# Performance work log

Measured on AMD Instinct MI355X. Metric: run time of the kernel, lower is better.

Reference implementation:

```python
import jax, jax.numpy as jnp
import numpy as np

CHUNK = 512  # tile size along N; keeps per-step [B,CHUNK,M] tile ~64 MB, never builds full [B,N,M]


def setup_inputs() -> dict:
    key = jax.random.key(0)
    k1, k2 = jax.random.split(key)
    xyz1 = jax.random.normal(k1, (4, 8192, 3), dtype=jnp.float32)
    xyz2 = jax.random.normal(k2, (4, 8192, 3), dtype=jnp.float32)
    return {"xyz1": xyz1, "xyz2": xyz2}


def _chamfer(xyz1, xyz2):
    # xyz1: [B,N,3], xyz2: [B,M,3]
    B, N, _ = xyz1.shape
    M = xyz2.shape[1]
    K = N // CHUNK
    x1_chunks = xyz1.reshape(B, K, CHUNK, 3).transpose(1, 0, 2, 3)  # [K,B,C,3]

    def step(carry, x1k):
        best_d2, best_i2, start = carry  # running mins for xyz2 -> xyz1 direction
        # squared distances for this tile: [B,C,M]
        d = jnp.sum((x1k[:, :, None, :] - xyz2[:, None, :, :]) ** 2, axis=-1)
        # xyz1 -> xyz2: min over M
        d1 = jnp.min(d, axis=2)                              # [B,C]
        i1 = jnp.argmin(d, axis=2).astype(jnp.int32)         # [B,C]
        # xyz2 -> xyz1: partial min over this chunk of N
        dc = jnp.min(d, axis=1)                              # [B,M]
        ic = jnp.argmin(d, axis=1).astype(jnp.int32) + start # [B,M], global index
        upd = dc < best_d2
        best_d2 = jnp.where(upd, dc, best_d2)
        best_i2 = jnp.where(upd, ic, best_i2)
        return (best_d2, best_i2, start + CHUNK), (d1, i1)

    init = (jnp.full((B, M), jnp.inf, dtype=xyz1.dtype),
            jnp.zeros((B, M), dtype=jnp.int32),
            jnp.int32(0))
    (dist2, idx2, _), (d1s, i1s) = jax.lax.scan(step, init, x1_chunks)
    dist1 = d1s.transpose(1, 0, 2).reshape(B, N)
    idx1 = i1s.transpose(1, 0, 2).reshape(B, N)
    return dist1, dist2, idx1, idx2


def reference(xyz1, xyz2):
    # Matches ChamferDistance.forward: (dist1, dist2, idx1, idx2),
    # squared nearest-neighbor distances and int32 argmin indices.
    return _chamfer(xyz1, xyz2)
```

## Files before the change

### kernel.cpp

```cpp
#include <hip/hip_runtime.h>
#include <math.h>


#define QPT 4
#define BLK 256
#define QPB (QPT*BLK)

__global__ __launch_bounds__(256, 4) void chamfer_main(
    const float* __restrict__ xyz1, const float* __restrict__ xyz2,
    unsigned long long* __restrict__ pp,
    int N, int M, int B, int S, int C)
{
    const int dir = blockIdx.z;
    const float* q = dir ? xyz2 : xyz1;
    const float* r = dir ? xyz1 : xyz2;
    const int Nq = dir ? M : N;
    const int Nr = dir ? N : M;
    const int b     = blockIdx.y / S;
    const int split = blockIdx.y % S;
    const int base  = split * C;

    extern __shared__ float s[];

    {
        const float4* gv = (const float4*)(r + ((size_t)b * Nr + base) * 3);
        float4* sv = (float4*)s;
        const int elems4 = C * 3 / 4;
        for (int t = threadIdx.x; t < elems4; t += BLK) sv[t] = gv[t];
    }
    __syncthreads();

    float qx[QPT], qy[QPT], qz[QPT];
    int qi[QPT];
    bool qv[QPT];
#pragma unroll
    for (int k = 0; k < QPT; ++k) {
        qi[k] = blockIdx.x * QPB + k * BLK + threadIdx.x;
        qv[k] = qi[k] < Nq;
        const float* qp = q + ((size_t)b * Nq + (qv[k] ? qi[k] : 0)) * 3;
        qx[k] = qp[0]; qy[k] = qp[1]; qz[k] = qp[2];
    }

    float bd[QPT];
    int   gi[QPT];
#pragma unroll
    for (int k = 0; k < QPT; ++k) { bd[k] = INFINITY; gi[k] = 0; }

    const float4* sv = (const float4*)s;
    const int iters = C / 8;
    for (int j8 = 0; j8 < iters; ++j8) {
        float4 f0 = sv[6 * j8 + 0];
        float4 f1 = sv[6 * j8 + 1];
        float4 f2 = sv[6 * j8 + 2];
        float4 f3 = sv[6 * j8 + 3];
        float4 f4 = sv[6 * j8 + 4];
        float4 f5 = sv[6 * j8 + 5];
        float px[8] = { f0.x, f0.w, f1.z, f2.y, f3.x, f3.w, f4.z, f5.y };
        float py[8] = { f0.y, f1.x, f1.w, f2.z, f3.y, f4.x, f4.w, f5.z };
        float pz[8] = { f0.z, f1.y, f2.x, f2.w, f3.z, f4.y, f5.x, f5.w };
#pragma unroll
        for (int k = 0; k < QPT; ++k) {
            float d[8];
#pragma unroll
            for (int p = 0; p < 8; ++p) {
                float dx = qx[k] - px[p];
                float dy = qy[k] - py[p];
                float dz = qz[k] - pz[p];
                d[p] = fmaf(dx, dx, fmaf(dy, dy, dz * dz));
            }
            float t0 = fminf(fminf(d[0], d[1]), d[2]);
            float t1 = fminf(fminf(d[3], d[4]), d[5]);
            float t2 = fminf(fminf(d[6], d[7]), t0);
            float m  = fminf(t1, t2);
            if (m < bd[k]) { bd[k] = m; gi[k] = j8; }
        }
    }

    const size_t obase = (size_t)(dir * B + b) * Nq;
    const int gbase = split * (C / 8);
#pragma unroll
    for (int k = 0; k < QPT; ++k) {
        if (!qv[k]) continue;
        unsigned long long packed =
            ((unsigned long long)__float_as_uint(bd[k]) << 32)
            | (unsigned)(gbase + gi[k]);
        atomicMin(&pp[obase + qi[k]], packed);
    }
}

__global__ __launch_bounds__(256) void chamfer_final(
    const float* __restrict__ xyz1, const float* __restrict__ xyz2,
    const unsigned long long* __restrict__ pp,
    float* __restrict__ out, int N, int M, int B)
{
    const int gid = blockIdx.x * blockDim.x + threadIdx.x;
    const int perDir0 = B * N;
    int dir, rem;
    if (gid < perDir0) { dir = 0; rem = gid; }
    else if (gid < perDir0 + B * M) { dir = 1; rem = gid - perDir0; }
    else return;
    const int Nq = dir ? M : N;
    const int Nr = dir ? N : M;
    const float* q = dir ? xyz2 : xyz1;
    const float* r = dir ? xyz1 : xyz2;

    unsigned long long v = pp[(size_t)(dir * B) * Nq + rem];
    const unsigned bits = (unsigned)(v >> 32);
    const int grp = (int)(v & 0xffffffffu);

    const int b  = rem / Nq;
    const int qi = rem - b * Nq;
    const float* qp = q + ((size_t)b * Nq + qi) * 3;
    const float qx = qp[0], qy = qp[1], qz = qp[2];

    const float4* rv = (const float4*)(r + ((size_t)b * Nr + (size_t)grp * 8) * 3);
    float4 f0 = rv[0], f1 = rv[1], f2 = rv[2], f3 = rv[3], f4 = rv[4], f5 = rv[5];
    float px[8] = { f0.x, f0.w, f1.z, f2.y, f3.x, f3.w, f4.z, f5.y };
    float py[8] = { f0.y, f1.x, f1.w, f2.z, f3.y, f4.x, f4.w, f5.z };
    float pz[8] = { f0.z, f1.y, f2.x, f2.w, f3.z, f4.y, f5.x, f5.w };
    int best = 0;
#pragma unroll
    for (int p = 7; p >= 0; --p) {
        float dx = qx - px[p];
        float dy = qy - py[p];
        float dz = qz - pz[p];
        float d = fmaf(dx, dx, fmaf(dy, dy, dz * dz));
        if (__float_as_uint(d) == bits) best = p;
    }
    const int idx = grp * 8 + best;

    float* dist_out = out + (dir ? (size_t)B * N : 0);
    float* idx_out  = out + (size_t)B * N + (size_t)B * M + (dir ? (size_t)B * N : 0);
    dist_out[rem] = __uint_as_float(bits);
    idx_out[rem]  = (float)idx;
}

extern "C" void kernel_launch(void* const* d_in, const int* in_sizes, int n_in,
                              void* d_out, int out_size, void* d_ws, size_t ws_size,
                              hipStream_t stream) {
    const float* xyz1 = (const float*)d_in[0];
    const float* xyz2 = (const float*)d_in[1];
    float* out = (float*)d_out;
    const int B = 4;
    const int N = in_sizes[0] / (B * 3);
    const int M = in_sizes[1] / (B * 3);
    const int NQ = (N > M ? N : M);
    const int NR = (N > M ? N : M);

    int S = 32;
    while (NR % (S * 8)) S >>= 1;
    const int C = NR / S;

    unsigned long long* pp = (unsigned long long*)d_ws;
    const int nslots = 2 * B * NQ;

    hipMemsetAsync(pp, 0xFF, (size_t)nslots * 8, stream);

    dim3 grid((NQ + QPB - 1) / QPB, B * S, 2);
    size_t lds = (size_t)C * 3 * sizeof(float);
    chamfer_main<<<grid, dim3(BLK, 1, 1), lds, stream>>>(
        xyz1, xyz2, pp, N, M, B, S, C);

    chamfer_final<<<dim3((nslots + 255) / 256, 1, 1), dim3(256, 1, 1), 0, stream>>>(
        xyz1, xyz2, pp, out, N, M, B);
}
```

Before: 122.6 us.

## Use expanded-norm distance form with exact rescan when candidates are ambiguous

The inner loop now computes distances as |r|^2 - 2 q·r, storing precomputed |r|^2 in the w lane of float4 LDS entries. This cuts per-pair arithmetic from about six ops to three FMAs. It tracks the best and second-best group minima. When the gap between them falls within an error bound, it rescans the tile and recomputes the candidate groups with exact differences. The winning group's distance is always recomputed exactly so results stay bit-matched, at the cost of a larger LDS footprint, extra registers and occasional rescans.

```diff
diff --git a/kernel.cpp b/kernel.cpp
--- a/kernel.cpp
+++ b/kernel.cpp
@@ -5,6 +5,51 @@
 #define QPT 4
 #define BLK 256
 #define QPB (QPT*BLK)
+
+#define LOADF8(J) do {                                                        \
+    f0 = sv4[8*(J)+0]; f1 = sv4[8*(J)+1]; f2 = sv4[8*(J)+2];                  \
+    f3 = sv4[8*(J)+3]; f4 = sv4[8*(J)+4]; f5 = sv4[8*(J)+5];                  \
+    f6 = sv4[8*(J)+6]; f7 = sv4[8*(J)+7];                                     \
+} while (0)
+
+#define EMIN8(AX, AY, AZ, MOUT) do {                                          \
+    float d0 = fmaf(AX, f0.x, fmaf(AY, f0.y, fmaf(AZ, f0.z, f0.w)));          \
+    float d1 = fmaf(AX, f1.x, fmaf(AY, f1.y, fmaf(AZ, f1.z, f1.w)));          \
+    float d2 = fmaf(AX, f2.x, fmaf(AY, f2.y, fmaf(AZ, f2.z, f2.w)));          \
+    float d3 = fmaf(AX, f3.x, fmaf(AY, f3.y, fmaf(AZ, f3.z, f3.w)));          \
+    float d4 = fmaf(AX, f4.x, fmaf(AY, f4.y, fmaf(AZ, f4.z, f4.w)));          \
+    float d5 = fmaf(AX, f5.x, fmaf(AY, f5.y, fmaf(AZ, f5.z, f5.w)));          \
+    float d6 = fmaf(AX, f6.x, fmaf(AY, f6.y, fmaf(AZ, f6.z, f6.w)));          \
+    float d7 = fmaf(AX, f7.x, fmaf(AY, f7.y, fmaf(AZ, f7.z, f7.w)));          \
+    float t0 = fminf(fminf(d0, d1), d2);                                      \
+    float t1 = fminf(fminf(d3, d4), d5);                                      \
+    float t2 = fminf(fminf(d6, d7), t0);                                      \
+    MOUT = fminf(t1, t2);                                                     \
+} while (0)
+
+#define DMIN8(QX, QY, QZ, MOUT) do {                                          \
+    float dx, dy, dz;                                                         \
+    dx = QX - f0.x; dy = QY - f0.y; dz = QZ - f0.z;                           \
+    float d0 = fmaf(dx, dx, fmaf(dy, dy, dz * dz));                           \
+    dx = QX - f1.x; dy = QY - f1.y; dz = QZ - f1.z;                           \
+    float d1 = fmaf(dx, dx, fmaf(dy, dy, dz * dz));                           \
+    dx = QX - f2.x; dy = QY - f2.y; dz = QZ - f2.z;                           \
+    float d2 = fmaf(dx, dx, fmaf(dy, dy, dz * dz));                           \
+    dx = QX - f3.x; dy = QY - f3.y; dz = QZ - f3.z;                           \
+    float d3 = fmaf(dx, dx, fmaf(dy, dy, dz * dz));                           \
+    dx = QX - f4.x; dy = QY - f4.y; dz = QZ - f4.z;                           \
+    float d4 = fmaf(dx, dx, fmaf(dy, dy, dz * dz));                           \
+    dx = QX - f5.x; dy = QY - f5.y; dz = QZ - f5.z;                           \
+    float d5 = fmaf(dx, dx, fmaf(dy, dy, dz * dz));                           \
+    dx = QX - f6.x; dy = QY - f6.y; dz = QZ - f6.z;                           \
+    float d6 = fmaf(dx, dx, fmaf(dy, dy, dz * dz));                           \
+    dx = QX - f7.x; dy = QY - f7.y; dz = QZ - f7.z;                           \
+    float d7 = fmaf(dx, dx, fmaf(dy, dy, dz * dz));                           \
+    float t0 = fminf(fminf(d0, d1), d2);                                      \
+    float t1 = fminf(fminf(d3, d4), d5);                                      \
+    float t2 = fminf(fminf(d6, d7), t0);                                      \
+    MOUT = fminf(t1, t2);                                                     \
+} while (0)
 
 __global__ __launch_bounds__(256, 4) void chamfer_main(
     const float* __restrict__ xyz1, const float* __restrict__ xyz2,
@@ -21,58 +66,49 @@
     const int base  = split * C;
 
     extern __shared__ float s[];
+    float4* sv4 = (float4*)s;
 
     {
-        const float4* gv = (const float4*)(r + ((size_t)b * Nr + base) * 3);
-        float4* sv = (float4*)s;
-        const int elems4 = C * 3 / 4;
-        for (int t = threadIdx.x; t < elems4; t += BLK) sv[t] = gv[t];
+        const float* g3 = r + ((size_t)b * Nr + base) * 3;
+        for (int t = threadIdx.x; t < C; t += BLK) {
+            float gx = g3[3 * t + 0];
+            float gy = g3[3 * t + 1];
+            float gz = g3[3 * t + 2];
+            float rr = fmaf(gz, gz, fmaf(gy, gy, gx * gx));
+            float4 f; f.x = gx; f.y = gy; f.z = gz; f.w = rr;
+            sv4[t] = f;
+        }
     }
     __syncthreads();
 
-    float qx[QPT], qy[QPT], qz[QPT];
+    float ax[QPT], ay[QPT], az[QPT];
     int qi[QPT];
-    bool qv[QPT];
+    bool qvv[QPT];
 #pragma unroll
     for (int k = 0; k < QPT; ++k) {
         qi[k] = blockIdx.x * QPB + k * BLK + threadIdx.x;
-        qv[k] = qi[k] < Nq;
-        const float* qp = q + ((size_t)b * Nq + (qv[k] ? qi[k] : 0)) * 3;
-        qx[k] = qp[0]; qy[k] = qp[1]; qz[k] = qp[2];
-    }
-
-    float bd[QPT];
-    int   gi[QPT];
-#pragma unroll
-    for (int k = 0; k < QPT; ++k) { bd[k] = INFINITY; gi[k] = 0; }
-
-    const float4* sv = (const float4*)s;
+        qvv[k] = qi[k] < Nq;
+        const float* qp = q + ((size_t)b * Nq + (qvv[k] ? qi[k] : 0)) * 3;
+        ax[k] = -2.0f * qp[0]; ay[k] = -2.0f * qp[1]; az[k] = -2.0f * qp[2];
+    }
+
+    float e1[QPT], e2[QPT];
+    int   g1[QPT];
+#pragma unroll
+    for (int k = 0; k < QPT; ++k) { e1[k] = INFINITY; e2[k] = INFINITY; g1[k] = 0; }
+
     const int iters = C / 8;
     for (int j8 = 0; j8 < iters; ++j8) {
-        float4 f0 = sv[6 * j8 + 0];
-        float4 f1 = sv[6 * j8 + 1];
-        float4 f2 = sv[6 * j8 + 2];
-        float4 f3 = sv[6 * j8 + 3];
-        float4 f4 = sv[6 * j8 + 4];
-        float4 f5 = sv[6 * j8 + 5];
-        float px[8] = { f0.x, f0.w, f1.z, f2.y, f3.x, f3.w, f4.z, f5.y };
-        float py[8] = { f0.y, f1.x, f1.w, f2.z, f3.y, f4.x, f4.w, f5.z };
-        float pz[8] = { f0.z, f1.y, f2.x, f2.w, f3.z, f4.y, f5.x, f5.w };
+        float4 f0, f1, f2, f3, f4, f5, f6, f7;
+        LOADF8(j8);
 #pragma unroll
         for (int k = 0; k < QPT; ++k) {
-            float d[8];
-#pragma unroll
-            for (int p = 0; p < 8; ++p) {
-                float dx = qx[k] - px[p];
-                float dy = qy[k] - py[p];
-                float dz = qz[k] - pz[p];
-                d[p] = fmaf(dx, dx, fmaf(dy, dy, dz * dz));
-            }
-            float t0 = fminf(fminf(d[0], d[1]), d[2]);
-            float t1 = fminf(fminf(d[3], d[4]), d[5]);
-            float t2 = fminf(fminf(d[6], d[7]), t0);
-            float m  = fminf(t1, t2);
-            if (m < bd[k]) { bd[k] = m; gi[k] = j8; }
+            float m;
+            EMIN8(ax[k], ay[k], az[k], m);
+            float h = fmaxf(e1[k], m);
+            e2[k] = fminf(e2[k], h);
+            if (m < e1[k]) g1[k] = j8;
+            e1[k] = fminf(e1[k], m);
         }
     }
 
@@ -80,10 +116,45 @@
     const int gbase = split * (C / 8);
 #pragma unroll
     for (int k = 0; k < QPT; ++k) {
-        if (!qv[k]) continue;
+        if (!qvv[k]) continue;
+        const float qx = -0.5f * ax[k], qy = -0.5f * ay[k], qz = -0.5f * az[k];
+        int gi = g1[k];
+        {
+            float qq  = fmaf(qx, qx, fmaf(qy, qy, qz * qz));
+            float d1e = qq + e1[k];
+            float rt  = sqrtf(qq) + sqrtf(fmaxf(d1e, 0.0f) + 0.01f);
+            float eps = 4e-6f * fmaf(2.0f, rt * rt, qq);
+            if (e2[k] - e1[k] <= eps) {
+                const float lim = e1[k] + eps;
+                unsigned long long mask = 0ull;
+                for (int j8 = 0; j8 < iters; ++j8) {
+                    float4 f0, f1, f2, f3, f4, f5, f6, f7;
+                    LOADF8(j8);
+                    float m;
+                    EMIN8(ax[k], ay[k], az[k], m);
+                    if (m <= lim) mask |= 1ull << j8;
+                }
+                float bdx = INFINITY; int gs = 0;
+                for (int j8 = 0; j8 < iters; ++j8) {
+                    if (!((mask >> j8) & 1)) continue;
+                    float4 f0, f1, f2, f3, f4, f5, f6, f7;
+                    LOADF8(j8);
+                    float md;
+                    DMIN8(qx, qy, qz, md);
+                    if (md < bdx) { bdx = md; gs = j8; }
+                }
+                gi = gs;
+            }
+        }
+        float m;
+        {
+            float4 f0, f1, f2, f3, f4, f5, f6, f7;
+            LOADF8(gi);
+            DMIN8(qx, qy, qz, m);
+        }
         unsigned long long packed =
-            ((unsigned long long)__float_as_uint(bd[k]) << 32)
-            | (unsigned)(gbase + gi[k]);
+            ((unsigned long long)__float_as_uint(m) << 32)
+            | (unsigned)(gbase + gi);
         atomicMin(&pp[obase + qi[k]], packed);
     }
 }
@@ -157,7 +228,7 @@
     hipMemsetAsync(pp, 0xFF, (size_t)nslots * 8, stream);
 
     dim3 grid((NQ + QPB - 1) / QPB, B * S, 2);
-    size_t lds = (size_t)C * 3 * sizeof(float);
+    size_t lds = (size_t)C * 4 * sizeof(float);
     chamfer_main<<<grid, dim3(BLK, 1, 1), lds, stream>>>(
         xyz1, xyz2, pp, N, M, B, S, C);
 
```

New measurement: 133.7 us. 9.0% more time.
